# Optimization experiments

Hardware: AMD Instinct MI355X
Metric: run time of the kernel (lower is better)

The kernel has to match this reference:

```python
import jax, jax.numpy as jnp
import numpy as np

D = 768

def _linear_params(key, name_idx, d_in, d_out):
    k1, k2 = jax.random.split(jax.random.fold_in(jax.random.key(42), name_idx))
    bound = 1.0 / np.sqrt(d_in)
    W = jax.random.uniform(k1, (d_out, d_in), jnp.float32, -bound, bound)
    b = jax.random.uniform(k2, (d_out,), jnp.float32, -bound, bound)
    return W, b

def setup_inputs() -> dict:
    key = jax.random.key(0)
    kq, kk, kv = jax.random.split(key, 3)
    B, S = 8, 2048
    inp = {
        'query': jax.random.normal(kq, (B, S, D), jnp.float32),
        'key': jax.random.normal(kk, (B, S, D), jnp.float32),
        'value': jax.random.normal(kv, (B, S, D), jnp.float32),
    }
    Wq, bq = _linear_params(key, 0, D, D)
    Wk, bk = _linear_params(key, 1, D, D)
    Wv, bv = _linear_params(key, 2, D, D)
    Wg1, bg1 = _linear_params(key, 3, D, D)
    Wg2, bg2 = _linear_params(key, 4, D, D)
    inp.update(Wq=Wq, bq=bq, Wk=Wk, bk=bk, Wv=Wv, bv=bv,
               Wg1=Wg1, bg1=bg1, Wg2=Wg2, bg2=bg2,
               text_scale=jnp.ones((1, D), jnp.float32))
    return inp

def reference(query, key, value, Wq, bq, Wk, bk, Wv, bv, Wg1, bg1, Wg2, bg2, text_scale):
    # Linear projections (torch Linear: x @ W.T + b)
    q = jnp.einsum('bsd,ed->bse', query, Wq) + bq
    k = jnp.einsum('bsd,ed->bse', key, Wk) + bk
    v = jnp.einsum('bsd,ed->bse', value, Wv) + bv
    scale = 1.0 / jnp.sqrt(jnp.float32(k.shape[-1]))
    scores = jnp.einsum('bqd,bkd->bqk', q, k) * scale  # [B, S, S]
    attn = jax.nn.softmax(scores, axis=-1)
    attended = jnp.einsum('bqk,bkd->bqd', attn, v)  # dropout = identity (eval)
    # text_gate: Linear -> ReLU -> Linear -> Sigmoid, then sigmoid applied AGAIN (faithful)
    h = jax.nn.relu(jnp.einsum('bsd,ed->bse', attended, Wg1) + bg1)
    gate = jax.nn.sigmoid(jnp.einsum('bsd,ed->bse', h, Wg2) + bg2)
    gated = jax.nn.sigmoid(gate) * attended * text_scale
    return gated
```

## Files before the change

kernel.cpp:

```cpp
#include <hip/hip_runtime.h>

typedef unsigned short ushort_t;
typedef __bf16 bf16x8 __attribute__((ext_vector_type(8)));
typedef float f32x4 __attribute__((ext_vector_type(4)));
typedef short short8 __attribute__((ext_vector_type(8)));

#define SBAR()   asm volatile("s_barrier" ::: "memory")
#define WAITV0() asm volatile("s_waitcnt vmcnt(0)" ::: "memory")
#define WAITV2() asm volatile("s_waitcnt vmcnt(2)" ::: "memory")
#define WAITV4() asm volatile("s_waitcnt vmcnt(4)" ::: "memory")
#define WAITV6() asm volatile("s_waitcnt vmcnt(6)" ::: "memory")
#define WAITL0() asm volatile("s_waitcnt lgkmcnt(0)" ::: "memory")

__device__ __forceinline__ float bf2f(unsigned short u) {
    union { unsigned int i; float f; } v; v.i = ((unsigned int)u) << 16; return v.f;
}
__device__ __forceinline__ unsigned short f2bf(float f) {
    union { float f; unsigned int i; } v; v.f = f;
    unsigned int r = v.i + 0x7fffu + ((v.i >> 16) & 1u);
    return (unsigned short)(r >> 16);
}
__device__ __forceinline__ float sigm(float x) { return 1.0f / (1.0f + __expf(-x)); }

__device__ __forceinline__ void async_copy16(const ushort_t* src, ushort_t* dst_lds) {
    __builtin_amdgcn_global_load_lds(
        (const __attribute__((address_space(1))) void*)src,
        (__attribute__((address_space(3))) void*)dst_lds,
        16, 0, 0);
}

#define WSEG 589824
#define NWALL 2949120
#define NTOT 2953728
__global__ __launch_bounds__(256)
void convert_params(const float* __restrict__ Wq, const float* __restrict__ Wk,
                    const float* __restrict__ Wv, const float* __restrict__ Wg1,
                    const float* __restrict__ Wg2, const float* __restrict__ bq,
                    const float* __restrict__ bk, const float* __restrict__ bv,
                    const float* __restrict__ bg1, const float* __restrict__ bg2,
                    const float* __restrict__ ts, ushort_t* __restrict__ dst)
{
    int i = (blockIdx.x * 256 + threadIdx.x) * 8;
    if (i >= NTOT) return;
    const float* src; int off;
    if (i < NWALL) {
        int wi = i / WSEG; off = i - wi * WSEG;
        src = (wi == 0) ? Wq : (wi == 1) ? Wk : (wi == 2) ? Wv : (wi == 3) ? Wg1 : Wg2;
    } else {
        int j = i - NWALL; int bi = j / 768; off = j - bi * 768;
        src = (bi == 0) ? bq : (bi == 1) ? bk : (bi == 2) ? bv : (bi == 3) ? bg1 : (bi == 4) ? bg2 : ts;
    }
    float4 a = *(const float4*)(src + off);
    float4 b = *(const float4*)(src + off + 4);
    short8 o;
    o[0] = (short)f2bf(a.x); o[1] = (short)f2bf(a.y); o[2] = (short)f2bf(a.z); o[3] = (short)f2bf(a.w);
    o[4] = (short)f2bf(b.x); o[5] = (short)f2bf(b.y); o[6] = (short)f2bf(b.z); o[7] = (short)f2bf(b.w);
    *(short8*)(dst + i) = o;
}

template<int EPI, int AF32, int CF32>
__global__ __launch_bounds__(256, 2)
void gemm_bt(const void* __restrict__ Av, const ushort_t* __restrict__ B,
             void* __restrict__ Cv, const ushort_t* __restrict__ bias,
             const ushort_t* __restrict__ aux, const ushort_t* __restrict__ ts,
             int M, int N, int K, float scale,
             long long batchA, long long batchB, long long batchC)
{
    __shared__ __align__(16) ushort_t As[2][128 * 32];
    __shared__ __align__(16) ushort_t Bs[2][128 * 32];
    const int tid  = threadIdx.x;
    const int lane = tid & 63;
    const int wave = tid >> 6;
    const int wr = wave >> 1, wc = wave & 1;

    const int gx = gridDim.x, gy = gridDim.y;
    const int nwg = gx * gy * gridDim.z;
    int fid = (blockIdx.z * gy + blockIdx.y) * gx + blockIdx.x;
    fid = (fid & 7) * (nwg >> 3) + (fid >> 3);
    const int bz  = fid / (gx * gy);
    const int rem = fid - bz * (gx * gy);
    const int by  = rem / gx;
    const int bx  = rem - by * gx;
    const int row0 = by * 128;
    const int col0 = bx * 128;

    f32x4 acc[4][4] = {};

    const int srow = tid >> 2;
    const int scol = (tid & 3) * 8;
    const ushort_t* ga0 = (const ushort_t*)Av + batchA * bz + (size_t)(row0 + srow) * K + scol;
    const ushort_t* gb0 = B + batchB * bz + (size_t)(col0 + srow) * K + scol;
    const int arow_s = tid >> 1;
    const int acol_s = (tid & 1) * 16;
    const float* gaf = (const float*)Av + batchA * bz + (size_t)(row0 + arow_s) * K + acol_s;

    const int kop  = (lane >> 4) * 8;
    const int arow = wr * 64 + (lane & 15);
    const int brow = wc * 64 + (lane & 15);

    const int NT = K >> 5;

    if (AF32) {
        float4 fa0 = *(const float4*)(gaf);
        float4 fa1 = *(const float4*)(gaf + 4);
        float4 fa2 = *(const float4*)(gaf + 8);
        float4 fa3 = *(const float4*)(gaf + 12);
        async_copy16(gb0,                  Bs[0] + tid * 8);
        async_copy16(gb0 + (size_t)64 * K, Bs[0] + 2048 + tid * 8);

        for (int t = 0; t < NT; ++t) {
            const int cur = t & 1;
            WAITV2();
            short8 p0, p1;
            p0[0] = (short)f2bf(fa0.x); p0[1] = (short)f2bf(fa0.y);
            p0[2] = (short)f2bf(fa0.z); p0[3] = (short)f2bf(fa0.w);
            p0[4] = (short)f2bf(fa1.x); p0[5] = (short)f2bf(fa1.y);
            p0[6] = (short)f2bf(fa1.z); p0[7] = (short)f2bf(fa1.w);
            p1[0] = (short)f2bf(fa2.x); p1[1] = (short)f2bf(fa2.y);
            p1[2] = (short)f2bf(fa2.z); p1[3] = (short)f2bf(fa2.w);
            p1[4] = (short)f2bf(fa3.x); p1[5] = (short)f2bf(fa3.y);
            p1[6] = (short)f2bf(fa3.z); p1[7] = (short)f2bf(fa3.w);
            *(short8*)(As[cur] + arow_s * 32 + acol_s)     = p0;
            *(short8*)(As[cur] + arow_s * 32 + acol_s + 8) = p1;
            if (t + 1 < NT) {
                const int k1 = (t + 1) * 32;
                fa0 = *(const float4*)(gaf + k1);
                fa1 = *(const float4*)(gaf + k1 + 4);
                fa2 = *(const float4*)(gaf + k1 + 8);
                fa3 = *(const float4*)(gaf + k1 + 12);
                async_copy16(gb0 + k1,                  Bs[cur ^ 1] + tid * 8);
                async_copy16(gb0 + (size_t)64 * K + k1, Bs[cur ^ 1] + 2048 + tid * 8);
                WAITV6();
            } else {
                WAITV0();
            }
            WAITL0();
            SBAR();
            bf16x8 af[4], bfr[4];
            #pragma unroll
            for (int m = 0; m < 4; ++m)
                af[m] = *(const bf16x8*)(As[cur] + (arow + m * 16) * 32 + kop);
            #pragma unroll
            for (int n = 0; n < 4; ++n)
                bfr[n] = *(const bf16x8*)(Bs[cur] + (brow + n * 16) * 32 + kop);
            #pragma unroll
            for (int m = 0; m < 4; ++m)
                #pragma unroll
                for (int n = 0; n < 4; ++n)
                    acc[m][n] = __builtin_amdgcn_mfma_f32_16x16x32_bf16(af[m], bfr[n], acc[m][n], 0, 0, 0);
            SBAR();
        }
    } else {
        async_copy16(ga0,                  As[0] + tid * 8);
        async_copy16(ga0 + (size_t)64 * K, As[0] + 2048 + tid * 8);
        async_copy16(gb0,                  Bs[0] + tid * 8);
        async_copy16(gb0 + (size_t)64 * K, Bs[0] + 2048 + tid * 8);

        for (int t = 0; t < NT; ++t) {
            const int cur = t & 1;
            if (t + 1 < NT) {
                const int k1 = (t + 1) * 32;
                async_copy16(ga0 + k1,                  As[cur ^ 1] + tid * 8);
                async_copy16(ga0 + (size_t)64 * K + k1, As[cur ^ 1] + 2048 + tid * 8);
                async_copy16(gb0 + k1,                  Bs[cur ^ 1] + tid * 8);
                async_copy16(gb0 + (size_t)64 * K + k1, Bs[cur ^ 1] + 2048 + tid * 8);
                WAITV4();
            } else {
                WAITV0();
            }
            SBAR();
            bf16x8 af[4], bfr[4];
            #pragma unroll
            for (int m = 0; m < 4; ++m)
                af[m] = *(const bf16x8*)(As[cur] + (arow + m * 16) * 32 + kop);
            #pragma unroll
            for (int n = 0; n < 4; ++n)
                bfr[n] = *(const bf16x8*)(Bs[cur] + (brow + n * 16) * 32 + kop);
            #pragma unroll
            for (int m = 0; m < 4; ++m)
                #pragma unroll
                for (int n = 0; n < 4; ++n)
                    acc[m][n] = __builtin_amdgcn_mfma_f32_16x16x32_bf16(af[m], bfr[n], acc[m][n], 0, 0, 0);
            SBAR();
        }
    }

    const int r0 = row0 + wr * 64 + (lane >> 4) * 4;
    const int c0 = col0 + wc * 64 + (lane & 15);
    #pragma unroll
    for (int m = 0; m < 4; ++m) {
        #pragma unroll
        for (int n = 0; n < 4; ++n) {
            const int col = c0 + n * 16;
            #pragma unroll
            for (int r = 0; r < 4; ++r) {
                const int row = r0 + m * 16 + r;
                float val = acc[m][n][r];
                if (EPI == 1) {
                    val += bf2f(bias[col]);
                } else if (EPI == 2) {
                    val *= scale;
                } else if (EPI == 3) {
                    val += bf2f(bias[col]);
                    val = fmaxf(val, 0.0f);
                } else if (EPI == 4) {
                    val += bf2f(bias[col]);
                    float g  = sigm(val);
                    float gg = sigm(g);
                    val = gg * bf2f(aux[batchC * bz + (size_t)row * N + col]) * bf2f(ts[col]);
                }
                if (CF32) ((float*)Cv)[batchC * bz + (size_t)row * N + col] = val;
                else      ((ushort_t*)Cv)[batchC * bz + (size_t)row * N + col] = f2bf(val);
            }
        }
    }
}

__global__ __launch_bounds__(256)
void softmax_inplace(ushort_t* __restrict__ P, int S)
{
    const size_t row = blockIdx.x;
    ushort_t* p = P + row * (size_t)S;
    const int tid = threadIdx.x;
    const int lane = tid & 63, wave = tid >> 6;

    short8 raw = *(const short8*)(p + tid * 8);
    float x[8];
    #pragma unroll
    for (int j = 0; j < 8; ++j) x[j] = bf2f((unsigned short)raw[j]);

    float mx = x[0];
    #pragma unroll
    for (int j = 1; j < 8; ++j) mx = fmaxf(mx, x[j]);
    #pragma unroll
    for (int o = 32; o > 0; o >>= 1) mx = fmaxf(mx, __shfl_xor(mx, o));
    __shared__ float redm[4], reds[4];
    if (lane == 0) redm[wave] = mx;
    __syncthreads();
    mx = fmaxf(fmaxf(redm[0], redm[1]), fmaxf(redm[2], redm[3]));

    float s = 0.f;
    #pragma unroll
    for (int j = 0; j < 8; ++j) { x[j] = __expf(x[j] - mx); s += x[j]; }
    #pragma unroll
    for (int o = 32; o > 0; o >>= 1) s += __shfl_xor(s, o);
    if (lane == 0) reds[wave] = s;
    __syncthreads();
    s = reds[0] + reds[1] + reds[2] + reds[3];
    const float inv = 1.0f / s;

    short8 outv;
    #pragma unroll
    for (int j = 0; j < 8; ++j) outv[j] = (short)f2bf(x[j] * inv);
    *(short8*)(p + tid * 8) = outv;
}

__global__ __launch_bounds__(256)
void transpose2d(const ushort_t* __restrict__ V, ushort_t* __restrict__ VT, int R, int Ccols)
{
    __shared__ ushort_t t[32][33];
    const size_t zoff = (size_t)blockIdx.z * R * Ccols;
    const int tx = threadIdx.x, ty = threadIdx.y;
    const int c = blockIdx.x * 32 + tx;
    const int rbase = blockIdx.y * 32;
    #pragma unroll
    for (int i = 0; i < 4; ++i)
        t[ty + i * 8][tx] = V[zoff + (size_t)(rbase + ty + i * 8) * Ccols + c];
    __syncthreads();
    const int r = rbase + tx;
    const int cbase = blockIdx.x * 32;
    #pragma unroll
    for (int i = 0; i < 4; ++i)
        VT[zoff + (size_t)(cbase + ty + i * 8) * R + r] = t[tx][ty + i * 8];
}

extern "C" void kernel_launch(void* const* d_in, const int* in_sizes, int n_in,
                              void* d_out, int out_size, void* d_ws, size_t ws_size,
                              hipStream_t stream)
{
    (void)in_sizes; (void)n_in; (void)out_size;
    const float* query = (const float*)d_in[0];
    const float* key_  = (const float*)d_in[1];
    const float* value = (const float*)d_in[2];
    const float* Wq  = (const float*)d_in[3];
    const float* bq  = (const float*)d_in[4];
    const float* Wk  = (const float*)d_in[5];
    const float* bk  = (const float*)d_in[6];
    const float* Wv  = (const float*)d_in[7];
    const float* bv  = (const float*)d_in[8];
    const float* Wg1 = (const float*)d_in[9];
    const float* bg1 = (const float*)d_in[10];
    const float* Wg2 = (const float*)d_in[11];
    const float* bg2 = (const float*)d_in[12];
    const float* tsc = (const float*)d_in[13];

    const int S = 2048, D = 768, Bc = 8;
    const int MS = Bc * S;
    const long long SD = (long long)S * D;
    const long long SS = (long long)S * S;

    char* ws = (char*)d_ws;
    ushort_t* q   = (ushort_t*)(ws);
    ushort_t* att = q;
    ushort_t* k   = (ushort_t*)(ws + 25165824ll);
    ushort_t* h   = k;
    ushort_t* vT  = (ushort_t*)(ws + 50331648ll);
    ushort_t* Wb  = (ushort_t*)(ws + 75497472ll);
    ushort_t* P   = (ushort_t*)(ws + 81404928ll);
    ushort_t* v   = (ushort_t*)d_out;

    const int WQ = 0, WK = 589824, WV = 1179648, WG1 = 1769472, WG2 = 2359296;
    const int BQ = 2949120, BK = 2949888, BV = 2950656, BG1 = 2951424, BG2 = 2952192, TSO = 2952960;

    const dim3 blk(256);
    const float scale = 0.03608439182435161f;
    const bool batched = ws_size >= 148513792ull;

    convert_params<<<dim3((NTOT / 8 + 255) / 256), blk, 0, stream>>>(
        Wq, Wk, Wv, Wg1, Wg2, bq, bk, bv, bg1, bg2, tsc, Wb);
    gemm_bt<1, 1, 0><<<dim3(D / 128, MS / 128), blk, 0, stream>>>(query, Wb + WQ, q, Wb + BQ, nullptr, nullptr, MS, D, D, 1.f, 0, 0, 0);
    gemm_bt<1, 1, 0><<<dim3(D / 128, MS / 128), blk, 0, stream>>>(key_,  Wb + WK, k, Wb + BK, nullptr, nullptr, MS, D, D, 1.f, 0, 0, 0);
    gemm_bt<1, 1, 0><<<dim3(D / 128, MS / 128), blk, 0, stream>>>(value, Wb + WV, v, Wb + BV, nullptr, nullptr, MS, D, D, 1.f, 0, 0, 0);
    transpose2d<<<dim3(D / 32, S / 32, Bc), dim3(32, 8), 0, stream>>>(v, vT, S, D);
    if (batched) {
        gemm_bt<2, 0, 0><<<dim3(S / 128, S / 128, Bc), blk, 0, stream>>>(q, k, P, nullptr, nullptr, nullptr, S, S, D, scale, SD, SD, SS);
        softmax_inplace<<<dim3(MS), blk, 0, stream>>>(P, S);
        gemm_bt<0, 0, 0><<<dim3(D / 128, S / 128, Bc), blk, 0, stream>>>(P, vT, att, nullptr, nullptr, nullptr, S, D, S, 1.f, SS, SD, SD);
    } else {
        for (int z = 0; z < Bc; ++z) {
            gemm_bt<2, 0, 0><<<dim3(S / 128, S / 128), blk, 0, stream>>>(q + (size_t)z * SD, k + (size_t)z * SD, P,
                                                                          nullptr, nullptr, nullptr, S, S, D, scale, 0, 0, 0);
            softmax_inplace<<<dim3(S), blk, 0, stream>>>(P, S);
            gemm_bt<0, 0, 0><<<dim3(D / 128, S / 128), blk, 0, stream>>>(P, vT + (size_t)z * SD, att + (size_t)z * SD,
                                                                          nullptr, nullptr, nullptr, S, D, S, 1.f, 0, 0, 0);
        }
    }
    gemm_bt<3, 0, 0><<<dim3(D / 128, MS / 128), blk, 0, stream>>>(att, Wb + WG1, h, Wb + BG1, nullptr, nullptr, MS, D, D, 1.f, 0, 0, 0);
    gemm_bt<4, 0, 1><<<dim3(D / 128, MS / 128), blk, 0, stream>>>(h, Wb + WG2, d_out, Wb + BG2, att, Wb + TSO, MS, D, D, 1.f, 0, 0, 0);
}
```

Baseline: 374.1 us.

## Fuse softmax into attention GEMMs and batch QKV projections in one launch

Removes the standalone softmax kernel. The QK^T GEMM epilogue now writes exp(score*scale) directly, and the PV GEMM accumulates row sums from its bf16 A fragments and normalizes in its epilogue. The three Q/K/V projection GEMMs are merged into one launch using the z grid dimension to select input, weight, bias and output. This saves a full read and write of the large score matrix plus several launches. In exchange it drops max-subtraction, so large scores could overflow, adds shuffle and VALU work to the PV GEMM main loop, and removes the small-workspace fallback path.

New measurement: 360.0 us. -3.8%, faster.

```diff
diff --git a/kernel.cpp b/kernel.cpp
--- a/kernel.cpp
+++ b/kernel.cpp
@@ -58,16 +58,19 @@
     *(short8*)(dst + i) = o;
 }
 
-template<int EPI, int AF32, int CF32>
+template<int EPI, int AF32, int CF32, int QKV>
 __global__ __launch_bounds__(256, 2)
-void gemm_bt(const void* __restrict__ Av, const ushort_t* __restrict__ B,
-             void* __restrict__ Cv, const ushort_t* __restrict__ bias,
+void gemm_bt(const void* __restrict__ Av, const void* __restrict__ Av1,
+             const void* __restrict__ Av2, const ushort_t* __restrict__ B,
+             void* __restrict__ Cv, void* __restrict__ Cv2,
+             const ushort_t* __restrict__ bias,
              const ushort_t* __restrict__ aux, const ushort_t* __restrict__ ts,
              int M, int N, int K, float scale,
              long long batchA, long long batchB, long long batchC)
 {
     __shared__ __align__(16) ushort_t As[2][128 * 32];
     __shared__ __align__(16) ushort_t Bs[2][128 * 32];
+    __shared__ float rs[128];
     const int tid  = threadIdx.x;
     const int lane = tid & 63;
     const int wave = tid >> 6;
@@ -85,6 +88,7 @@
     const int col0 = bx * 128;
 
     f32x4 acc[4][4] = {};
+    float psum[4] = {0.f, 0.f, 0.f, 0.f};
 
     const int srow = tid >> 2;
     const int scol = (tid & 3) * 8;
@@ -92,7 +96,9 @@
     const ushort_t* gb0 = B + batchB * bz + (size_t)(col0 + srow) * K + scol;
     const int arow_s = tid >> 1;
     const int acol_s = (tid & 1) * 16;
-    const float* gaf = (const float*)Av + batchA * bz + (size_t)(row0 + arow_s) * K + acol_s;
+    const float* gafb = (const float*)Av;
+    if (QKV) gafb = (bz == 0) ? (const float*)Av : (bz == 1) ? (const float*)Av1 : (const float*)Av2;
+    const float* gaf = gafb + (QKV ? 0 : batchA * bz) + (size_t)(row0 + arow_s) * K + acol_s;
 
     const int kop  = (lane >> 4) * 8;
     const int arow = wr * 64 + (lane & 15);
@@ -181,10 +187,39 @@
                 #pragma unroll
                 for (int n = 0; n < 4; ++n)
                     acc[m][n] = __builtin_amdgcn_mfma_f32_16x16x32_bf16(af[m], bfr[n], acc[m][n], 0, 0, 0);
+            if (EPI == 6) {
+                #pragma unroll
+                for (int m = 0; m < 4; ++m) {
+                    short8 u = __builtin_bit_cast(short8, af[m]);
+                    float s = bf2f((unsigned short)u[0]) + bf2f((unsigned short)u[1])
+                            + bf2f((unsigned short)u[2]) + bf2f((unsigned short)u[3])
+                            + bf2f((unsigned short)u[4]) + bf2f((unsigned short)u[5])
+                            + bf2f((unsigned short)u[6]) + bf2f((unsigned short)u[7]);
+                    s += __shfl_xor(s, 16);
+                    s += __shfl_xor(s, 32);
+                    psum[m] += s;
+                }
+            }
             SBAR();
         }
     }
 
+    float rinv[4][4];
+    if (EPI == 6) {
+        if (wc == 0 && lane < 16) {
+            #pragma unroll
+            for (int m = 0; m < 4; ++m) rs[wr * 64 + m * 16 + lane] = psum[m];
+        }
+        __syncthreads();
+        #pragma unroll
+        for (int m = 0; m < 4; ++m)
+            #pragma unroll
+            for (int r = 0; r < 4; ++r)
+                rinv[m][r] = 1.0f / rs[wr * 64 + m * 16 + (lane >> 4) * 4 + r];
+    }
+
+    ushort_t* Cb = (QKV && bz == 2) ? (ushort_t*)Cv2 : (ushort_t*)Cv + batchC * bz;
+    float* Cf = (float*)Cv;
     const int r0 = row0 + wr * 64 + (lane >> 4) * 4;
     const int c0 = col0 + wc * 64 + (lane & 15);
     #pragma unroll
@@ -197,7 +232,7 @@
                 const int row = r0 + m * 16 + r;
                 float val = acc[m][n][r];
                 if (EPI == 1) {
-                    val += bf2f(bias[col]);
+                    val += bf2f(bias[(QKV ? bz * 768 : 0) + col]);
                 } else if (EPI == 2) {
                     val *= scale;
                 } else if (EPI == 3) {
@@ -207,52 +242,17 @@
                     val += bf2f(bias[col]);
                     float g  = sigm(val);
                     float gg = sigm(g);
-                    val = gg * bf2f(aux[batchC * bz + (size_t)row * N + col]) * bf2f(ts[col]);
+                    val = gg * bf2f(aux[(size_t)row * N + col]) * bf2f(ts[col]);
+                } else if (EPI == 5) {
+                    val = __expf(val * scale);
+                } else if (EPI == 6) {
+                    val *= rinv[m][r];
                 }
-                if (CF32) ((float*)Cv)[batchC * bz + (size_t)row * N + col] = val;
-                else      ((ushort_t*)Cv)[batchC * bz + (size_t)row * N + col] = f2bf(val);
+                if (CF32) Cf[(size_t)row * N + col] = val;
+                else      Cb[(size_t)row * N + col] = f2bf(val);
             }
         }
     }
-}
-
-__global__ __launch_bounds__(256)
-void softmax_inplace(ushort_t* __restrict__ P, int S)
-{
-    const size_t row = blockIdx.x;
-    ushort_t* p = P + row * (size_t)S;
-    const int tid = threadIdx.x;
-    const int lane = tid & 63, wave = tid >> 6;
-
-    short8 raw = *(const short8*)(p + tid * 8);
-    float x[8];
-    #pragma unroll
-    for (int j = 0; j < 8; ++j) x[j] = bf2f((unsigned short)raw[j]);
-
-    float mx = x[0];
-    #pragma unroll
-    for (int j = 1; j < 8; ++j) mx = fmaxf(mx, x[j]);
-    #pragma unroll
-    for (int o = 32; o > 0; o >>= 1) mx = fmaxf(mx, __shfl_xor(mx, o));
-    __shared__ float redm[4], reds[4];
-    if (lane == 0) redm[wave] = mx;
-    __syncthreads();
-    mx = fmaxf(fmaxf(redm[0], redm[1]), fmaxf(redm[2], redm[3]));
-
-    float s = 0.f;
-    #pragma unroll
-    for (int j = 0; j < 8; ++j) { x[j] = __expf(x[j] - mx); s += x[j]; }
-    #pragma unroll
-    for (int o = 32; o > 0; o >>= 1) s += __shfl_xor(s, o);
-    if (lane == 0) reds[wave] = s;
-    __syncthreads();
-    s = reds[0] + reds[1] + reds[2] + reds[3];
-    const float inv = 1.0f / s;
-
-    short8 outv;
-    #pragma unroll
-    for (int j = 0; j < 8; ++j) outv[j] = (short)f2bf(x[j] * inv);
-    *(short8*)(p + tid * 8) = outv;
 }
 
 __global__ __launch_bounds__(256)
@@ -278,7 +278,7 @@
                               void* d_out, int out_size, void* d_ws, size_t ws_size,
                               hipStream_t stream)
 {
-    (void)in_sizes; (void)n_in; (void)out_size;
+    (void)in_sizes; (void)n_in; (void)out_size; (void)ws_size;
     const float* query = (const float*)d_in[0];
     const float* key_  = (const float*)d_in[1];
     const float* value = (const float*)d_in[2];
@@ -298,6 +298,7 @@
     const int MS = Bc * S;
     const long long SD = (long long)S * D;
     const long long SS = (long long)S * S;
+    const long long MSD = (long long)MS * D;
 
     char* ws = (char*)d_ws;
     ushort_t* q   = (ushort_t*)(ws);
@@ -305,36 +306,32 @@
     ushort_t* k   = (ushort_t*)(ws + 25165824ll);
     ushort_t* h   = k;
     ushort_t* vT  = (ushort_t*)(ws + 50331648ll);
-    ushort_t* Wb  = (ushort_t*)(ws + 75497472ll);
-    ushort_t* P   = (ushort_t*)(ws + 81404928ll);
+    ushort_t* P   = (ushort_t*)(ws + 75497472ll);
+    ushort_t* Wb  = (ushort_t*)(ws + 142606336ll);
     ushort_t* v   = (ushort_t*)d_out;
 
-    const int WQ = 0, WK = 589824, WV = 1179648, WG1 = 1769472, WG2 = 2359296;
-    const int BQ = 2949120, BK = 2949888, BV = 2950656, BG1 = 2951424, BG2 = 2952192, TSO = 2952960;
+    const int WQ = 0, WG1 = 1769472, WG2 = 2359296;
+    const int BQ = 2949120, BG1 = 2951424, BG2 = 2952192, TSO = 2952960;
 
     const dim3 blk(256);
     const float scale = 0.03608439182435161f;
-    const bool batched = ws_size >= 148513792ull;
 
     convert_params<<<dim3((NTOT / 8 + 255) / 256), blk, 0, stream>>>(
         Wq, Wk, Wv, Wg1, Wg2, bq, bk, bv, bg1, bg2, tsc, Wb);
-    gemm_bt<1, 1, 0><<<dim3(D / 128, MS / 128), blk, 0, stream>>>(query, Wb + WQ, q, Wb + BQ, nullptr, nullptr, MS, D, D, 1.f, 0, 0, 0);
-    gemm_bt<1, 1, 0><<<dim3(D / 128, MS / 128), blk, 0, stream>>>(key_,  Wb + WK, k, Wb + BK, nullptr, nullptr, MS, D, D, 1.f, 0, 0, 0);
-    gemm_bt<1, 1, 0><<<dim3(D / 128, MS / 128), blk, 0, stream>>>(value, Wb + WV, v, Wb + BV, nullptr, nullptr, MS, D, D, 1.f, 0, 0, 0);
+    gemm_bt<1, 1, 0, 1><<<dim3(D / 128, MS / 128, 3), blk, 0, stream>>>(
+        query, key_, value, Wb + WQ, q, v, Wb + BQ, nullptr, nullptr,
+        MS, D, D, 1.f, 0, (long long)WSEG, MSD);
     transpose2d<<<dim3(D / 32, S / 32, Bc), dim3(32, 8), 0, stream>>>(v, vT, S, D);
-    if (batched) {
-        gemm_bt<2, 0, 0><<<dim3(S / 128, S / 128, Bc), blk, 0, stream>>>(q, k, P, nullptr, nullptr, nullptr, S, S, D, scale, SD, SD, SS);
-        softmax_inplace<<<dim3(MS), blk, 0, stream>>>(P, S);
-        gemm_bt<0, 0, 0><<<dim3(D / 128, S / 128, Bc), blk, 0, stream>>>(P, vT, att, nullptr, nullptr, nullptr, S, D, S, 1.f, SS, SD, SD);
-    } else {
-        for (int z = 0; z < Bc; ++z) {
-            gemm_bt<2, 0, 0><<<dim3(S / 128, S / 128), blk, 0, stream>>>(q + (size_t)z * SD, k + (size_t)z * SD, P,
-                                                                          nullptr, nullptr, nullptr, S, S, D, scale, 0, 0, 0);
-            softmax_inplace<<<dim3(S), blk, 0, stream>>>(P, S);
-            gemm_bt<0, 0, 0><<<dim3(D / 128, S / 128), blk, 0, stream>>>(P, vT + (size_t)z * SD, att + (size_t)z * SD,
-                                                                          nullptr, nullptr, nullptr, S, D, S, 1.f, 0, 0, 0);
-        }
-    }
-    gemm_bt<3, 0, 0><<<dim3(D / 128, MS / 128), blk, 0, stream>>>(att, Wb + WG1, h, Wb + BG1, nullptr, nullptr, MS, D, D, 1.f, 0, 0, 0);
-    gemm_bt<4, 0, 1><<<dim3(D / 128, MS / 128), blk, 0, stream>>>(h, Wb + WG2, d_out, Wb + BG2, att, Wb + TSO, MS, D, D, 1.f, 0, 0, 0);
-}
+    gemm_bt<5, 0, 0, 0><<<dim3(S / 128, S / 128, Bc), blk, 0, stream>>>(
+        q, nullptr, nullptr, k, P, nullptr, nullptr, nullptr, nullptr,
+        S, S, D, scale, SD, SD, SS);
+    gemm_bt<6, 0, 0, 0><<<dim3(D / 128, S / 128, Bc), blk, 0, stream>>>(
+        P, nullptr, nullptr, vT, att, nullptr, nullptr, nullptr, nullptr,
+        S, D, S, 1.f, SS, SD, SD);
+    gemm_bt<3, 0, 0, 0><<<dim3(D / 128, MS / 128, 1), blk, 0, stream>>>(
+        att, nullptr, nullptr, Wb + WG1, h, nullptr, Wb + BG1, nullptr, nullptr,
+        MS, D, D, 1.f, 0, 0, 0);
+    gemm_bt<4, 0, 1, 0><<<dim3(D / 128, MS / 128, 1), blk, 0, stream>>>(
+        h, nullptr, nullptr, Wb + WG2, d_out, nullptr, Wb + BG2, att, Wb + TSO,
+        MS, D, D, 1.f, 0, 0, 0);
+}
```
